# Kernel tuning notes

Hardware: AMD Instinct MI355X
Metric: run time of the kernel (lower is better)

## Reference

```python
import jax, jax.numpy as jnp
import numpy as np

LN_EPS = 1e-5
LEAKY_SLOPE = 0.2

B, N_FEAT = 512, 8192
N_GROUPS, G, D = 512, 64, 128


def setup_inputs() -> dict:
    key = jax.random.key(0)
    k1, k2, k3 = jax.random.split(key, 3)
    x = jax.random.normal(k1, (B, N_FEAT), dtype=jnp.float32)
    idx = jax.random.randint(k2, (N_GROUPS, G), 0, N_FEAT)
    # per-group Linear weights, scaled like torch default init ~U(-1/sqrt(fan_in),...)
    W = jax.random.normal(k3, (N_GROUPS, G, D), dtype=jnp.float32) / jnp.sqrt(jnp.float32(G))
    b = jnp.zeros((N_GROUPS, D), dtype=jnp.float32)
    gamma = jnp.ones((D,), dtype=jnp.float32)   # shared LayerNorm affine (single nn.LayerNorm)
    beta = jnp.zeros((D,), dtype=jnp.float32)
    return {"x": x, "idx": idx, "W": W, "b": b, "gamma": gamma, "beta": beta}


def reference(x, idx, W, b, gamma, beta):
    # Gather each group's feature subset: [B, n_groups, G]
    xg = x[:, idx]
    # Grouped (block-diagonal) GEMM: per-group Linear -> [B, n_groups, D]
    h = jnp.einsum('bng,ngd->bnd', xg, W) + b
    # LeakyReLU(0.2)
    h = jnp.where(h >= 0, h, LEAKY_SLOPE * h)
    # Shared LayerNorm over last dim
    mu = jnp.mean(h, axis=-1, keepdims=True)
    c = h - mu
    var = jnp.mean(c * c, axis=-1, keepdims=True)
    out = c * jax.lax.rsqrt(var + LN_EPS) * gamma + beta
    # dropout treated as identity (deterministic/eval reference)
    return out  # matches torch.stack(output, dim=1): [B, n_groups, D]
```

## Files before the change

kernel.cpp:

```cpp
#include <hip/hip_runtime.h>
#include <stdint.h>

#define NB 512
#define NFEAT 8192
#define NG 512
#define GG 64
#define DD 128

typedef short bf16x8 __attribute__((ext_vector_type(8)));
typedef float f32x4 __attribute__((ext_vector_type(4)));
typedef unsigned int u32x4 __attribute__((ext_vector_type(4)));
typedef unsigned short u16;

__device__ __forceinline__ u16 f2bf(float f) {
  unsigned u = __builtin_bit_cast(unsigned, f);
  u += 0x7FFFu + ((u >> 16) & 1u);
  return (u16)(u >> 16);
}

__global__ __launch_bounds__(256) void prep_fused(const float* __restrict__ x,
                                                  u16* __restrict__ xTb,
                                                  const float* __restrict__ W,
                                                  u16* __restrict__ Wt) {
  __shared__ __attribute__((aligned(16))) char lds[18432];
  const int bid = blockIdx.x;
  const int tid = threadIdx.x;
  if (bid < 1024) {
    float (*t)[65] = (float (*)[65])lds;
    const int c0 = (bid & 127) * 64;
    const int b0 = (bid >> 7) * 64;
    const int col = tid & 63;
    const int rg = tid >> 6;
    #pragma unroll
    for (int r = 0; r < 16; ++r) {
      int row = rg * 16 + r;
      t[col][row] = x[(size_t)(b0 + row) * NFEAT + c0 + col];
    }
    __syncthreads();
    #pragma unroll
    for (int r = 0; r < 16; ++r) {
      int crow = rg * 16 + r;
      xTb[(size_t)(c0 + crow) * NB + b0 + col] = f2bf(t[crow][col]);
    }
  } else {
    u16 (*tl)[GG + 8] = (u16 (*)[GG + 8])lds;
    const int n = bid - 1024;
    const float* wn = W + (size_t)n * (GG * DD);
    #pragma unroll
    for (int i = 0; i < 32; ++i) {
      int e = i * 256 + tid;
      int g = e >> 7, d = e & 127;
      tl[d][g] = f2bf(wn[e]);
    }
    __syncthreads();
    u16* dst = Wt + (size_t)n * (DD * GG);
    const int d = tid >> 1, gh = (tid & 1) * 32;
    #pragma unroll
    for (int k = 0; k < 32; ++k)
      dst[d * GG + gh + k] = tl[d][gh + k];
  }
}

__global__ __launch_bounds__(256) void lc_mfma(
    const u16* __restrict__ xTb,
    const u16* __restrict__ Wt,
    const int* __restrict__ idx,
    const float* __restrict__ bias,
    const float* __restrict__ gamma,
    const float* __restrict__ beta,
    float* __restrict__ out) {
  const int n = blockIdx.y;
  const int b0 = blockIdx.x * 128;
  const int tid = threadIdx.x;
  const int lane = tid & 63;
  const int w = tid >> 6;
  const int q = lane >> 4;
  const int lm = lane & 15;
  const int bb = b0 + w * 32;

  const int* idxn = idx + n * GG;

  int cof[16];
  #pragma unroll
  for (int ks = 0; ks < 2; ++ks)
    #pragma unroll
    for (int j = 0; j < 8; ++j)
      cof[ks * 8 + j] = idxn[ks * 32 + q * 8 + j] * NB;

  bf16x8 afr[2][2];
  #pragma unroll
  for (int mi = 0; mi < 2; ++mi) {
    const int arow = bb + mi * 16 + lm;
    #pragma unroll
    for (int ks = 0; ks < 2; ++ks) {
      unsigned p[4];
      #pragma unroll
      for (int r = 0; r < 4; ++r) {
        unsigned t0 = xTb[cof[ks * 8 + 2 * r]     + arow];
        unsigned t1 = xTb[cof[ks * 8 + 2 * r + 1] + arow];
        p[r] = t0 | (t1 << 16);
      }
      u32x4 a4; a4.x = p[0]; a4.y = p[1]; a4.z = p[2]; a4.w = p[3];
      afr[ks][mi] = __builtin_bit_cast(bf16x8, a4);
    }
  }

  const u16* wtn = Wt + (size_t)n * (DD * GG);
  f32x4 acc[2][8];
  #pragma unroll
  for (int mi = 0; mi < 2; ++mi)
    #pragma unroll
    for (int ni = 0; ni < 8; ++ni) acc[mi][ni] = f32x4{0.f, 0.f, 0.f, 0.f};

  #pragma unroll
  for (int ks = 0; ks < 2; ++ks) {
    #pragma unroll
    for (int ni = 0; ni < 8; ++ni) {
      const int d = ni * 16 + lm;
      bf16x8 bfr = *(const bf16x8*)(wtn + d * GG + ks * 32 + q * 8);
      acc[0][ni] = __builtin_amdgcn_mfma_f32_16x16x32_bf16(afr[ks][0], bfr, acc[0][ni], 0, 0, 0);
      acc[1][ni] = __builtin_amdgcn_mfma_f32_16x16x32_bf16(afr[ks][1], bfr, acc[1][ni], 0, 0, 0);
    }
  }

  float bv[8], gv[8], tv[8];
  #pragma unroll
  for (int ni = 0; ni < 8; ++ni) {
    const int d = ni * 16 + lm;
    bv[ni] = bias[n * DD + d];
    gv[ni] = gamma[d];
    tv[ni] = beta[d];
  }
  #pragma unroll
  for (int mi = 0; mi < 2; ++mi) {
    #pragma unroll
    for (int r = 0; r < 4; ++r) {
      float h[8];
      float s = 0.f, s2 = 0.f;
      #pragma unroll
      for (int ni = 0; ni < 8; ++ni) {
        float v = acc[mi][ni][r] + bv[ni];
        v = (v >= 0.f) ? v : 0.2f * v;
        h[ni] = v;
        s += v;
        s2 += v * v;
      }
      s  += __shfl_xor(s, 1);  s  += __shfl_xor(s, 2);
      s  += __shfl_xor(s, 4);  s  += __shfl_xor(s, 8);
      s2 += __shfl_xor(s2, 1); s2 += __shfl_xor(s2, 2);
      s2 += __shfl_xor(s2, 4); s2 += __shfl_xor(s2, 8);
      const float mu = s * (1.f / 128.f);
      const float var = s2 * (1.f / 128.f) - mu * mu;
      const float rs = rsqrtf(var + 1e-5f);

      const int brow = bb + mi * 16 + q * 4 + r;
      float* ob = out + ((size_t)brow * NG + n) * DD + lm;
      #pragma unroll
      for (int ni = 0; ni < 8; ++ni)
        __builtin_nontemporal_store((h[ni] - mu) * rs * gv[ni] + tv[ni], ob + ni * 16);
    }
  }
}

extern "C" void kernel_launch(void* const* d_in, const int* in_sizes, int n_in,
                              void* d_out, int out_size, void* d_ws, size_t ws_size,
                              hipStream_t stream) {
  const float* x     = (const float*)d_in[0];
  const int*   idx   = (const int*)d_in[1];
  const float* W     = (const float*)d_in[2];
  const float* bias  = (const float*)d_in[3];
  const float* gamma = (const float*)d_in[4];
  const float* beta  = (const float*)d_in[5];
  float* out = (float*)d_out;

  u16* xTb = (u16*)d_ws;
  u16* Wt  = xTb + (size_t)NFEAT * NB;

  prep_fused<<<1536, 256, 0, stream>>>(x, xTb, W, Wt);
  lc_mfma<<<dim3(NB / 128, NG), 256, 0, stream>>>(xTb, Wt, idx, bias, gamma, beta, out);
}
```

Before: 59.74 us.

## Vectorize prep stores, remap blocks per XCD, and vector-load group indices

The transpose-to-bf16 store now packs two bf16 values per 32-bit store, and the W transpose writes 16-byte vectors from LDS instead of scalar u16 stores. The main kernel uses a 1D grid and remaps block IDs so blocks that share a group land on the same XCD, which should improve L2 reuse of Wt and the gathered x rows. The idx loads also become int4 vector loads. Together these aim to cut store-instruction count and cross-XCD cache misses, at the cost of slightly more complex indexing.

Result: faster. 55.84 us (-6.5%).

```diff
diff --git a/kernel.cpp b/kernel.cpp
--- a/kernel.cpp
+++ b/kernel.cpp
@@ -37,10 +37,14 @@
       t[col][row] = x[(size_t)(b0 + row) * NFEAT + c0 + col];
     }
     __syncthreads();
+    const int sc = tid & 31;
+    const int srg = tid >> 5;
     #pragma unroll
-    for (int r = 0; r < 16; ++r) {
-      int crow = rg * 16 + r;
-      xTb[(size_t)(c0 + crow) * NB + b0 + col] = f2bf(t[crow][col]);
+    for (int r = 0; r < 8; ++r) {
+      int crow = srg * 8 + r;
+      unsigned px = (unsigned)f2bf(t[crow][2 * sc]) |
+                    ((unsigned)f2bf(t[crow][2 * sc + 1]) << 16);
+      *(unsigned*)(xTb + (size_t)(c0 + crow) * NB + b0 + 2 * sc) = px;
     }
   } else {
     u16 (*tl)[GG + 8] = (u16 (*)[GG + 8])lds;
@@ -55,9 +59,13 @@
     __syncthreads();
     u16* dst = Wt + (size_t)n * (DD * GG);
     const int d = tid >> 1, gh = (tid & 1) * 32;
-    #pragma unroll
-    for (int k = 0; k < 32; ++k)
-      dst[d * GG + gh + k] = tl[d][gh + k];
+    const u16* src = &tl[d][gh];
+    u32x4 v0 = *(const u32x4*)(src);
+    u32x4 v1 = *(const u32x4*)(src + 8);
+    u32x4 v2 = *(const u32x4*)(src + 16);
+    u32x4 v3 = *(const u32x4*)(src + 24);
+    u32x4* dp = (u32x4*)(dst + d * GG + gh);
+    dp[0] = v0; dp[1] = v1; dp[2] = v2; dp[3] = v3;
   }
 }
 
@@ -69,8 +77,11 @@
     const float* __restrict__ gamma,
     const float* __restrict__ beta,
     float* __restrict__ out) {
-  const int n = blockIdx.y;
-  const int b0 = blockIdx.x * 128;
+  const int lin = blockIdx.x;
+  const int xcd = lin & 7;
+  const int slot = lin >> 3;
+  const int n = (slot & 63) * 8 + xcd;
+  const int b0 = (slot >> 6) * 128;
   const int tid = threadIdx.x;
   const int lane = tid & 63;
   const int w = tid >> 6;
@@ -82,10 +93,14 @@
 
   int cof[16];
   #pragma unroll
-  for (int ks = 0; ks < 2; ++ks)
-    #pragma unroll
-    for (int j = 0; j < 8; ++j)
-      cof[ks * 8 + j] = idxn[ks * 32 + q * 8 + j] * NB;
+  for (int ks = 0; ks < 2; ++ks) {
+    int4 ca = *(const int4*)(idxn + ks * 32 + q * 8);
+    int4 cb = *(const int4*)(idxn + ks * 32 + q * 8 + 4);
+    cof[ks * 8 + 0] = ca.x * NB; cof[ks * 8 + 1] = ca.y * NB;
+    cof[ks * 8 + 2] = ca.z * NB; cof[ks * 8 + 3] = ca.w * NB;
+    cof[ks * 8 + 4] = cb.x * NB; cof[ks * 8 + 5] = cb.y * NB;
+    cof[ks * 8 + 6] = cb.z * NB; cof[ks * 8 + 7] = cb.w * NB;
+  }
 
   bf16x8 afr[2][2];
   #pragma unroll
@@ -177,5 +192,5 @@
   u16* Wt  = xTb + (size_t)NFEAT * NB;
 
   prep_fused<<<1536, 256, 0, stream>>>(x, xTb, W, Wt);
-  lc_mfma<<<dim3(NB / 128, NG), 256, 0, stream>>>(xTb, Wt, idx, bias, gamma, beta, out);
+  lc_mfma<<<2048, 256, 0, stream>>>(xTb, Wt, idx, bias, gamma, beta, out);
 }
```
